# Optimization experiments

Measured on AMD Instinct MI355X. Metric: run time of the kernel, lower is better.

Reference implementation:

```python
import jax, jax.numpy as jnp
import numpy as np
from jax import lax

BLOCKS, LAYERS = 2, 10
RES_CH, DL_CH, OUT_CH, IN_CH, K = 32, 32, 256, 1, 2
B, L = 4, 65536
W_SCALE = 0.05


def conv1d(x, w, b, dilation=1, padding=0):
    # x: [B, Cin, L], w: [Cout, Cin, K], b: [Cout]
    out = lax.conv_general_dilated(
        x, w, window_strides=(1,), padding=[(padding, padding)],
        rhs_dilation=(dilation,), dimension_numbers=('NCH', 'OIH', 'NCH'))
    return out + b[None, :, None]


def setup_inputs() -> dict:
    key = jax.random.key(0)
    ks = jax.random.split(key, 16)
    n = lambda k, shp: jax.random.normal(k, shp, dtype=jnp.float32) * W_SCALE
    inp = {
        'x': jax.random.normal(ks[0], (B, IN_CH, L), dtype=jnp.float32),
        'w_start': n(ks[1], (RES_CH, IN_CH, 1)),
        'b_start': n(ks[2], (RES_CH,)),
        # per-block, per-layer stacked params
        'filt_w': n(ks[3], (BLOCKS, LAYERS, DL_CH, RES_CH, K)),
        'filt_b': n(ks[4], (BLOCKS, LAYERS, DL_CH)),
        'gate_w': n(ks[5], (BLOCKS, LAYERS, DL_CH, RES_CH, K)),
        'gate_b': n(ks[6], (BLOCKS, LAYERS, DL_CH)),
        'res_w': n(ks[7], (BLOCKS, LAYERS, RES_CH, DL_CH, 1)),
        'res_b': n(ks[8], (BLOCKS, LAYERS, RES_CH)),
        'skip_w': n(ks[9], (BLOCKS, LAYERS, RES_CH, DL_CH, 1)),
        'skip_b': n(ks[10], (BLOCKS, LAYERS, RES_CH)),
        'w_end1': n(ks[11], (OUT_CH, RES_CH, 1)),
        'b_end1': n(ks[12], (OUT_CH,)),
        'w_end2': n(ks[13], (OUT_CH, OUT_CH, 1)),
        'b_end2': n(ks[14], (OUT_CH,)),
    }
    return inp


def reference(x, w_start, b_start, filt_w, filt_b, gate_w, gate_b,
              res_w, res_b, skip_w, skip_b, w_end1, b_end1, w_end2, b_end2):
    resid = conv1d(x, w_start, b_start)                    # [B, RES_CH, L]
    skip_total = jnp.zeros_like(resid)
    for blk in range(BLOCKS):
        r = resid
        skip = jnp.zeros_like(r)
        dilation = 1
        for i in range(LAYERS):
            pad = 1 if i == 0 else dilation * (K - 1) // 2
            f = conv1d(r, filt_w[blk, i], filt_b[blk, i], dilation, pad)
            g = conv1d(r, gate_w[blk, i], gate_b[blk, i], dilation, pad)
            if i == 0:  # source slices off the extra trailing sample
                f = f[:, :, :-1]
                g = g[:, :, :-1]
            layer_out = f * g  # NOTE: original forward applies no tanh/sigmoid
            skip = skip + conv1d(layer_out, skip_w[blk, i], skip_b[blk, i])
            r = r + conv1d(layer_out, res_w[blk, i], res_b[blk, i])
            dilation *= 2
        resid = r
        skip_total = skip_total + skip
    out = jax.nn.relu(skip_total)
    out = jax.nn.relu(conv1d(out, w_end1, b_end1))         # [B, OUT_CH, L]
    return conv1d(out, w_end2, b_end2)
```

## Files before the change

kernel.cpp:

```cpp
#include <hip/hip_runtime.h>

typedef unsigned short ushort_t;
typedef __attribute__((ext_vector_type(8))) short bf16x8;
typedef __attribute__((ext_vector_type(4))) float f32x4;

#define NTOK 262144

__device__ __forceinline__ float bf2f(ushort_t u) {
    union { unsigned u; float f; } v; v.u = ((unsigned)u) << 16; return v.f;
}
__device__ __forceinline__ ushort_t f2bf(float f) {
    union { float f; unsigned u; } v; v.f = f;
    unsigned r = 0x7fffu + ((v.u >> 16) & 1u);
    return (ushort_t)((v.u + r) >> 16);
}
__device__ __forceinline__ float ldany(const void* p, long i, int isf32) {
    return isf32 ? ((const float*)p)[i] : bf2f(((const ushort_t*)p)[i]);
}
__device__ __forceinline__ bf16x8 zero8() {
    bf16x8 z = {0,0,0,0,0,0,0,0}; return z;
}
__device__ __forceinline__ void mm3(f32x4& acc, bf16x8 ah, bf16x8 al,
                                    bf16x8 bh, bf16x8 bl) {
    acc = __builtin_amdgcn_mfma_f32_16x16x32_bf16(ah, bh, acc, 0, 0, 0);
    acc = __builtin_amdgcn_mfma_f32_16x16x32_bf16(ah, bl, acc, 0, 0, 0);
    acc = __builtin_amdgcn_mfma_f32_16x16x32_bf16(al, bh, acc, 0, 0, 0);
}
__device__ __forceinline__ void loD2B(f32x4 lo0, f32x4 lo1, int l15, int l4,
                                      bf16x8& bh, bf16x8& bl) {
    #pragma unroll
    for (int j = 0; j < 8; j++) {
        int src = l15 + (((2 * l4 + (j >> 2)) & 3) << 4);
        float v0 = __shfl(lo0[j & 3], src);
        float v1 = __shfl(lo1[j & 3], src);
        float v = (l4 < 2) ? v0 : v1;
        ushort_t h = f2bf(v);
        bh[j] = (short)h;
        bl[j] = (short)f2bf(v - bf2f(h));
    }
}

#define OFF_FB  122880
#define OFF_GB  123520
#define OFF_RB  124160
#define OFF_SB  124800
#define OFF_WST 125440
#define OFF_BST 125472
#define OFF_B1  133696
#define OFF_B2  199488
#define OFF_FLAG 199744
#define SKIP_OFF 262144
#define OFF_W2AH 8650752
#define OFF_W2AL 8683520
#define OFF_W1AH 8716288
#define OFF_W1AL 8720384
#define OFF_FGW  8724480
#define OFF_GGW  8765440
#define OFF_RWH  8806400
#define OFF_SWH  8826880

__device__ __forceinline__ char* rchunk(void* outb, int buf, int b) {
    return (char*)outb + (((long)buf * 32 + (long)b * 8) << 20);
}

__global__ void k_convert(const void* fw, const void* fb,
                          const void* gw, const void* gb,
                          const void* rw, const void* rb,
                          const void* sw, const void* sb,
                          const void* wst, const void* bst,
                          const void* w1, const void* b1,
                          const void* w2, const void* b2,
                          float* W) {
    __shared__ int sh;
    if (threadIdx.x == 0) sh = 0;
    __syncthreads();
    {
        const ushort_t* p = (const ushort_t*)fw;
        int f = 0;
        for (int j = 0; j < 16; j++) {
            ushort_t u = p[threadIdx.x * 16 + j];
            f |= (((u >> 7) & 0xFF) == 0xFF) ? 1 : 0;
        }
        if (f) atomicOr(&sh, 1);
    }
    __syncthreads();
    const int isf32 = sh;
    if (blockIdx.x == 0 && threadIdx.x == 0) W[OFF_FLAG] = (float)isf32;

    int tid = blockIdx.x * blockDim.x + threadIdx.x;
    int stride = gridDim.x * blockDim.x;

    ushort_t* fgp = (ushort_t*)(W + OFF_FGW);
    ushort_t* ggp = (ushort_t*)(W + OFF_GGW);
    ushort_t* rwp = (ushort_t*)(W + OFF_RWH);
    ushort_t* swp = (ushort_t*)(W + OFF_SWH);
    for (int idx = tid; idx < 20480; idx += stride) {
        int wl = idx >> 10;
        int coci = idx & 1023;
        #pragma unroll
        for (int tap = 0; tap < 2; tap++) {
            long base = (long)wl * 4096 + tap * 2048 + coci;
            float v = ldany(fw, (long)idx * 2 + tap, isf32);
            ushort_t h = f2bf(v);
            fgp[base] = h; fgp[base + 1024] = f2bf(v - bf2f(h));
            v = ldany(gw, (long)idx * 2 + tap, isf32);
            h = f2bf(v);
            ggp[base] = h; ggp[base + 1024] = f2bf(v - bf2f(h));
        }
        {
            long base = (long)wl * 2048 + coci;
            float v = ldany(rw, idx, isf32);
            ushort_t h = f2bf(v);
            rwp[base] = h; rwp[base + 1024] = f2bf(v - bf2f(h));
            v = ldany(sw, idx, isf32);
            h = f2bf(v);
            swp[base] = h; swp[base + 1024] = f2bf(v - bf2f(h));
        }
    }
    for (int idx = tid; idx < 640; idx += stride) {
        W[OFF_FB + idx] = ldany(fb, idx, isf32);
        W[OFF_GB + idx] = ldany(gb, idx, isf32);
        W[OFF_RB + idx] = ldany(rb, idx, isf32);
        W[OFF_SB + idx] = ldany(sb, idx, isf32);
    }
    for (int idx = tid; idx < 32; idx += stride) {
        W[OFF_WST + idx] = ldany(wst, idx, isf32);
        W[OFF_BST + idx] = ldany(bst, idx, isf32);
    }
    for (int idx = tid; idx < 256; idx += stride) {
        W[OFF_B1 + idx] = ldany(b1, idx, isf32);
        W[OFF_B2 + idx] = ldany(b2, idx, isf32);
    }
    {
        ushort_t* w2h = (ushort_t*)(W + OFF_W2AH);
        ushort_t* w2l = (ushort_t*)(W + OFF_W2AL);
        for (int idx = tid; idx < 65536; idx += stride) {
            float v = ldany(w2, idx, isf32);
            ushort_t h = f2bf(v);
            w2h[idx] = h;
            w2l[idx] = f2bf(v - bf2f(h));
        }
        ushort_t* w1h = (ushort_t*)(W + OFF_W1AH);
        ushort_t* w1l = (ushort_t*)(W + OFF_W1AL);
        for (int idx = tid; idx < 8192; idx += stride) {
            float v = ldany(w1, idx, isf32);
            ushort_t h = f2bf(v);
            w1h[idx] = h;
            w1l[idx] = f2bf(v - bf2f(h));
        }
    }
}

__global__ __launch_bounds__(256) void k_init(const void* __restrict__ x,
                                              const float* __restrict__ W,
                                              void* __restrict__ outb,
                                              float* __restrict__ skp) {
    int tid = blockIdx.x * blockDim.x + threadIdx.x;
    int b = tid >> 16, l = tid & 65535;
    const int isf32 = (W[OFF_FLAG] > 0.5f) ? 1 : 0;
    float xv = ldany(x, tid, isf32);
    union { uint4 q[4]; unsigned w[16]; } H, L;
    #pragma unroll
    for (int c2 = 0; c2 < 16; c2++) {
        float v0 = W[OFF_WST + c2*2]     * xv + W[OFF_BST + c2*2];
        float v1 = W[OFF_WST + c2*2 + 1] * xv + W[OFF_BST + c2*2 + 1];
        ushort_t h0 = f2bf(v0), h1 = f2bf(v1);
        H.w[c2] = (unsigned)h0 | ((unsigned)h1 << 16);
        L.w[c2] = (unsigned)f2bf(v0 - bf2f(h0)) |
                  ((unsigned)f2bf(v1 - bf2f(h1)) << 16);
    }
    uint4* rp = (uint4*)(rchunk(outb, 0, b) + (long)l * 128);
    #pragma unroll
    for (int q = 0; q < 4; q++) { rp[q] = H.q[q]; rp[4 + q] = L.q[q]; }
    float* sg = skp + ((long)b << 21) + (long)l * 32;
    f32x4 z = {0.f, 0.f, 0.f, 0.f};
    #pragma unroll
    for (int j = 0; j < 8; j++) *(f32x4*)(sg + j * 4) = z;
}

template<int NTW>
__global__ __launch_bounds__(256) void k_pair(const float* __restrict__ W,
                                              void* __restrict__ outb,
                                              float* __restrict__ skp,
                                              int bufin, int bufout,
                                              int wlX, int t0X, int t1X, int TY) {
    constexpr int RTOK = NTW * 64;
    constexpr int RH = NTW * 32 - 128;
    __shared__ __align__(16) char r1[RTOK * 128];
    __shared__ __align__(16) char sxs[256 * 128];
    const int tid = threadIdx.x;
    const int lane = tid & 63;
    const int wv = tid >> 6;
    const int l15 = lane & 15;
    const int l4 = lane >> 4;
    const int b = blockIdx.x >> 8;
    const int lbase = (blockIdx.x & 255) << 8;

    const char* __restrict__ rin = rchunk(outb, bufin, b);
    char* __restrict__ rout      = rchunk(outb, bufout, b);

    {
        const ushort_t* __restrict__ FG  = (const ushort_t*)(W + OFF_FGW) + (long)wlX * 4096;
        const ushort_t* __restrict__ GG  = (const ushort_t*)(W + OFF_GGW) + (long)wlX * 4096;
        const ushort_t* __restrict__ RWH = (const ushort_t*)(W + OFF_RWH) + (long)wlX * 2048;
        const ushort_t* __restrict__ SWH = (const ushort_t*)(W + OFF_SWH) + (long)wlX * 2048;
        bf16x8 afh[2][2], afl[2][2], agh[2][2], agl[2][2];
        #pragma unroll
        for (int tap = 0; tap < 2; tap++)
            #pragma unroll
            for (int mt = 0; mt < 2; mt++) {
                int row = (mt * 16 + l15) * 32 + l4 * 8;
                afh[tap][mt] = *(const bf16x8*)(FG + tap * 2048 + row);
                afl[tap][mt] = *(const bf16x8*)(FG + tap * 2048 + 1024 + row);
                agh[tap][mt] = *(const bf16x8*)(GG + tap * 2048 + row);
                agl[tap][mt] = *(const bf16x8*)(GG + tap * 2048 + 1024 + row);
            }
        bf16x8 ash[2], asl2[2], arh[2], arl[2];
        #pragma unroll
        for (int mt = 0; mt < 2; mt++) {
            int row = (mt * 16 + l15) * 32 + l4 * 8;
            ash[mt]  = *(const bf16x8*)(SWH + row);
            asl2[mt] = *(const bf16x8*)(SWH + 1024 + row);
            arh[mt]  = *(const bf16x8*)(RWH + row);
            arl[mt]  = *(const bf16x8*)(RWH + 1024 + row);
        }
        f32x4 fb2[2], gb2[2], sb4[2], rb4[2];
        #pragma unroll
        for (int mt = 0; mt < 2; mt++) {
            fb2[mt] = *(const f32x4*)(W + OFF_FB + wlX * 32 + mt * 16 + l4 * 4);
            gb2[mt] = *(const f32x4*)(W + OFF_GB + wlX * 32 + mt * 16 + l4 * 4);
            sb4[mt] = *(const f32x4*)(W + OFF_SB + wlX * 32 + mt * 16 + l4 * 4);
            rb4[mt] = *(const f32x4*)(W + OFF_RB + wlX * 32 + mt * 16 + l4 * 4);
        }
        const int offs[2] = {t0X, t1X};
        for (int it = 0; it < NTW; it++) {
            const int rt = wv * NTW + it;
            const int tokl = lbase - RH + rt * 16 + l15;
            f32x4 fa[2] = {fb2[0], fb2[1]};
            f32x4 ga[2] = {gb2[0], gb2[1]};
            #pragma unroll
            for (int tap = 0; tap < 2; tap++) {
                int lt = tokl + offs[tap];
                bf16x8 bh = zero8(), bl = zero8();
                if ((unsigned)lt < 65536u) {
                    const char* rp = rin + (long)lt * 128 + l4 * 16;
                    bh = *(const bf16x8*)rp;
                    bl = *(const bf16x8*)(rp + 64);
                }
                #pragma unroll
                for (int mt = 0; mt < 2; mt++) {
                    mm3(fa[mt], afh[tap][mt], afl[tap][mt], bh, bl);
                    mm3(ga[mt], agh[tap][mt], agl[tap][mt], bh, bl);
                }
            }
            bf16x8 pbh, pbl;
            loD2B(fa[0] * ga[0], fa[1] * ga[1], l15, l4, pbh, pbl);
            f32x4 rdv[2] = {rb4[0], rb4[1]};
            mm3(rdv[0], arh[0], arl[0], pbh, pbl);
            mm3(rdv[1], arh[1], arl[1], pbh, pbl);
            const int reltok = rt * 16 + l15;
            uint2 rxh[2] = {{0u,0u},{0u,0u}}, rxl[2] = {{0u,0u},{0u,0u}};
            if ((unsigned)tokl < 65536u) {
                const char* rp = rin + (long)tokl * 128 + l4 * 8;
                rxh[0] = *(const uint2*)(rp);
                rxh[1] = *(const uint2*)(rp + 32);
                rxl[0] = *(const uint2*)(rp + 64);
                rxl[1] = *(const uint2*)(rp + 96);
            }
            const int sw = (reltok & 7) << 4;
            #pragma unroll
            for (int mt = 0; mt < 2; mt++) {
                float v0 = bf2f((ushort_t)(rxh[mt].x & 0xffffu)) + bf2f((ushort_t)(rxl[mt].x & 0xffffu)) + rdv[mt][0];
                float v1 = bf2f((ushort_t)(rxh[mt].x >> 16))     + bf2f((ushort_t)(rxl[mt].x >> 16))     + rdv[mt][1];
                float v2 = bf2f((ushort_t)(rxh[mt].y & 0xffffu)) + bf2f((ushort_t)(rxl[mt].y & 0xffffu)) + rdv[mt][2];
                float v3 = bf2f((ushort_t)(rxh[mt].y >> 16))     + bf2f((ushort_t)(rxl[mt].y >> 16))     + rdv[mt][3];
                ushort_t h0 = f2bf(v0), h1 = f2bf(v1), h2 = f2bf(v2), h3 = f2bf(v3);
                uint2 ph, pl;
                ph.x = (unsigned)h0 | ((unsigned)h1 << 16);
                ph.y = (unsigned)h2 | ((unsigned)h3 << 16);
                pl.x = (unsigned)f2bf(v0 - bf2f(h0)) | ((unsigned)f2bf(v1 - bf2f(h1)) << 16);
                pl.y = (unsigned)f2bf(v2 - bf2f(h2)) | ((unsigned)f2bf(v3 - bf2f(h3)) << 16);
                *(uint2*)(r1 + ((reltok * 128 + mt * 32 + l4 * 8) ^ sw)) = ph;
                *(uint2*)(r1 + ((reltok * 128 + 64 + mt * 32 + l4 * 8) ^ sw)) = pl;
            }
            const int rel0 = rt * 16 - RH;
            if (rel0 >= 0 && rel0 < 256) {
                f32x4 sd0 = sb4[0], sd1 = sb4[1];
                mm3(sd0, ash[0], asl2[0], pbh, pbl);
                mm3(sd1, ash[1], asl2[1], pbh, pbl);
                const int ct = rel0 + l15;
                const int sws = (ct & 7) << 4;
                *(f32x4*)(sxs + ((ct * 128 + l4 * 16) ^ sws)) = sd0;
                *(f32x4*)(sxs + ((ct * 128 + 64 + l4 * 16) ^ sws)) = sd1;
            }
        }
    }
    __syncthreads();

    {
        const int wlY = wlX + 1;
        const ushort_t* __restrict__ FG  = (const ushort_t*)(W + OFF_FGW) + (long)wlY * 4096;
        const ushort_t* __restrict__ GG  = (const ushort_t*)(W + OFF_GGW) + (long)wlY * 4096;
        const ushort_t* __restrict__ RWH = (const ushort_t*)(W + OFF_RWH) + (long)wlY * 2048;
        const ushort_t* __restrict__ SWH = (const ushort_t*)(W + OFF_SWH) + (long)wlY * 2048;
        bf16x8 afh[2][2], afl[2][2], agh[2][2], agl[2][2];
        #pragma unroll
        for (int tap = 0; tap < 2; tap++)
            #pragma unroll
            for (int mt = 0; mt < 2; mt++) {
                int row = (mt * 16 + l15) * 32 + l4 * 8;
                afh[tap][mt] = *(const bf16x8*)(FG + tap * 2048 + row);
                afl[tap][mt] = *(const bf16x8*)(FG + tap * 2048 + 1024 + row);
                agh[tap][mt] = *(const bf16x8*)(GG + tap * 2048 + row);
                agl[tap][mt] = *(const bf16x8*)(GG + tap * 2048 + 1024 + row);
            }
        bf16x8 ash[2], asl2[2], arh[2], arl[2];
        #pragma unroll
        for (int mt = 0; mt < 2; mt++) {
            int row = (mt * 16 + l15) * 32 + l4 * 8;
            ash[mt]  = *(const bf16x8*)(SWH + row);
            asl2[mt] = *(const bf16x8*)(SWH + 1024 + row);
            arh[mt]  = *(const bf16x8*)(RWH + row);
            arl[mt]  = *(const bf16x8*)(RWH + 1024 + row);
        }
        f32x4 fb2[2], gb2[2], sb4[2], rb4[2];
        #pragma unroll
        for (int mt = 0; mt < 2; mt++) {
            fb2[mt] = *(const f32x4*)(W + OFF_FB + wlY * 32 + mt * 16 + l4 * 4);
            gb2[mt] = *(const f32x4*)(W + OFF_GB + wlY * 32 + mt * 16 + l4 * 4);
            sb4[mt] = *(const f32x4*)(W + OFF_SB + wlY * 32 + mt * 16 + l4 * 4);
            rb4[mt] = *(const f32x4*)(W + OFF_RB + wlY * 32 + mt * 16 + l4 * 4);
        }
        #pragma unroll
        for (int it = 0; it < 4; it++) {
            const int tt = wv * 64 + it * 16 + l15;
            const int tokg = lbase + tt;
            f32x4 fa[2] = {fb2[0], fb2[1]};
            f32x4 ga[2] = {gb2[0], gb2[1]};
            #pragma unroll
            for (int tap = 0; tap < 2; tap++) {
                int dd = tap ? TY : -TY;
                int tg = tokg + dd;
                bf16x8 bh = zero8(), bl = zero8();
                if ((unsigned)tg < 65536u) {
                    int rel = tt + dd + RH;
                    int sw = (rel & 7) << 4;
                    bh = *(const bf16x8*)(r1 + ((rel * 128 + l4 * 16) ^ sw));
                    bl = *(const bf16x8*)(r1 + ((rel * 128 + 64 + l4 * 16) ^ sw));
                }
                #pragma unroll
                for (int mt = 0; mt < 2; mt++) {
                    mm3(fa[mt], afh[tap][mt], afl[tap][mt], bh, bl);
                    mm3(ga[mt], agh[tap][mt], agl[tap][mt], bh, bl);
                }
            }
            bf16x8 pbh, pbl;
            loD2B(fa[0] * ga[0], fa[1] * ga[1], l15, l4, pbh, pbl);
            f32x4 sd0 = sb4[0], sd1 = sb4[1];
            mm3(sd0, ash[0], asl2[0], pbh, pbl);
            mm3(sd1, ash[1], asl2[1], pbh, pbl);
            f32x4 rdv[2] = {rb4[0], rb4[1]};
            mm3(rdv[0], arh[0], arl[0], pbh, pbl);
            mm3(rdv[1], arh[1], arl[1], pbh, pbl);
            {
                const int swc = (tt & 7) << 4;
                f32x4 sx0 = *(const f32x4*)(sxs + ((tt * 128 + l4 * 16) ^ swc));
                f32x4 sx1 = *(const f32x4*)(sxs + ((tt * 128 + 64 + l4 * 16) ^ swc));
                float* sg = skp + ((long)b << 21) + (long)tokg * 32 + l4 * 4;
                *(f32x4*)sg        = *(const f32x4*)sg        + (sd0 + sx0);
                *(f32x4*)(sg + 16) = *(const f32x4*)(sg + 16) + (sd1 + sx1);
            }
            const int relc = tt + RH;
            const int swr = (relc & 7) << 4;
            #pragma unroll
            for (int mt = 0; mt < 2; mt++) {
                uint2 h  = *(const uint2*)(r1 + ((relc * 128 + mt * 32 + l4 * 8) ^ swr));
                uint2 lo = *(const uint2*)(r1 + ((relc * 128 + 64 + mt * 32 + l4 * 8) ^ swr));
                float v0 = bf2f((ushort_t)(h.x & 0xffffu)) + bf2f((ushort_t)(lo.x & 0xffffu)) + rdv[mt][0];
                float v1 = bf2f((ushort_t)(h.x >> 16))     + bf2f((ushort_t)(lo.x >> 16))     + rdv[mt][1];
                float v2 = bf2f((ushort_t)(h.y & 0xffffu)) + bf2f((ushort_t)(lo.y & 0xffffu)) + rdv[mt][2];
                float v3 = bf2f((ushort_t)(h.y >> 16))     + bf2f((ushort_t)(lo.y >> 16))     + rdv[mt][3];
                ushort_t h0 = f2bf(v0), h1 = f2bf(v1), h2 = f2bf(v2), h3 = f2bf(v3);
                uint2 ph, pl;
                ph.x = (unsigned)h0 | ((unsigned)h1 << 16);
                ph.y = (unsigned)h2 | ((unsigned)h3 << 16);
                pl.x = (unsigned)f2bf(v0 - bf2f(h0)) | ((unsigned)f2bf(v1 - bf2f(h1)) << 16);
                pl.y = (unsigned)f2bf(v2 - bf2f(h2)) | ((unsigned)f2bf(v3 - bf2f(h3)) << 16);
                char* op = rout + (long)tokg * 128 + mt * 32 + l4 * 8;
                *(uint2*)op        = ph;
                *(uint2*)(op + 64) = pl;
            }
        }
    }
}

__global__ __launch_bounds__(512, 4) void k_final(const float* __restrict__ W,
                                                  const float* __restrict__ skp,
                                                  void* __restrict__ outv) {
    __shared__ ushort_t h1s[128 * 256];
    const int tid = threadIdx.x;
    const int lane = tid & 63;
    const int wv = tid >> 6;
    const int wm = wv & 3;
    const int wn = wv >> 2;
    const int l15 = lane & 15;
    const int l4 = lane >> 4;
    const int isf32 = (W[OFF_FLAG] > 0.5f) ? 1 : 0;
    const int tokbase = blockIdx.x * 128 + wn * 64;

    const ushort_t* __restrict__ W1AH = (const ushort_t*)(W + OFF_W1AH);
    const ushort_t* __restrict__ W1AL = (const ushort_t*)(W + OFF_W1AL);
    const ushort_t* __restrict__ W2AH = (const ushort_t*)(W + OFF_W2AH);
    const ushort_t* __restrict__ W2AL = (const ushort_t*)(W + OFF_W2AL);

    bf16x8 bhi[4], blo[4];
    #pragma unroll
    for (int nt = 0; nt < 4; nt++) {
        int tok = tokbase + nt * 16 + l15;
        int bb = tok >> 16, ll = tok & 65535;
        const float* __restrict__ sk = skp + ((long)bb << 21) + (long)ll * 32 + l4 * 8;
        f32x4 u0 = *(const f32x4*)(sk);
        f32x4 u1 = *(const f32x4*)(sk + 4);
        bf16x8 h, o_;
        #pragma unroll
        for (int j = 0; j < 8; j++) {
            float v = (j < 4) ? u0[j] : u1[j - 4];
            v = v > 0.f ? v : 0.f;
            ushort_t hh = f2bf(v);
            h[j] = (short)hh;
            o_[j] = (short)f2bf(v - bf2f(hh));
        }
        bhi[nt] = h; blo[nt] = o_;
    }

    #pragma unroll
    for (int mt = 0; mt < 4; mt++) {
        int o0 = wm * 64 + mt * 16;
        const bf16x8 a_hi = *(const bf16x8*)(W1AH + (o0 + l15) * 32 + l4 * 8);
        const bf16x8 a_lo = *(const bf16x8*)(W1AL + (o0 + l15) * 32 + l4 * 8);
        f32x4 bias;
        #pragma unroll
        for (int r = 0; r < 4; r++) bias[r] = W[OFF_B1 + o0 + l4 * 4 + r];
        #pragma unroll
        for (int nt = 0; nt < 4; nt++) {
            f32x4 acc = bias;
            acc = __builtin_amdgcn_mfma_f32_16x16x32_bf16(a_hi, bhi[nt], acc, 0, 0, 0);
            acc = __builtin_amdgcn_mfma_f32_16x16x32_bf16(a_hi, blo[nt], acc, 0, 0, 0);
            acc = __builtin_amdgcn_mfma_f32_16x16x32_bf16(a_lo, bhi[nt], acc, 0, 0, 0);
            int ltk = wn * 64 + nt * 16 + l15;
            int ci0 = o0 + l4 * 4;
            float v0 = acc[0] > 0.f ? acc[0] : 0.f;
            float v1 = acc[1] > 0.f ? acc[1] : 0.f;
            float v2 = acc[2] > 0.f ? acc[2] : 0.f;
            float v3 = acc[3] > 0.f ? acc[3] : 0.f;
            uint2 pk;
            pk.x = (unsigned)f2bf(v0) | ((unsigned)f2bf(v1) << 16);
            pk.y = (unsigned)f2bf(v2) | ((unsigned)f2bf(v3) << 16);
            int byteoff = (ltk << 9) + (ci0 << 1);
            byteoff ^= (ltk & 7) << 4;
            *(uint2*)((char*)h1s + byteoff) = pk;
        }
    }
    __syncthreads();

    f32x4 acc[4][4];
    #pragma unroll
    for (int mt = 0; mt < 4; mt++) {
        int m0 = wm * 64 + mt * 16 + l4 * 4;
        #pragma unroll
        for (int r = 0; r < 4; r++) {
            float bv = W[OFF_B2 + m0 + r];
            #pragma unroll
            for (int nt = 0; nt < 4; nt++) acc[mt][nt][r] = bv;
        }
    }
    #pragma unroll 2
    for (int ks = 0; ks < 8; ks++) {
        bf16x8 bf[4];
        #pragma unroll
        for (int nt = 0; nt < 4; nt++) {
            int ltk = wn * 64 + nt * 16 + l15;
            int byteoff = (ltk << 9) + (ks << 6) + (l4 << 4);
            byteoff ^= (ltk & 7) << 4;
            bf[nt] = *(const bf16x8*)((const char*)h1s + byteoff);
        }
        #pragma unroll
        for (int mt = 0; mt < 4; mt++) {
            int o = wm * 64 + mt * 16 + l15;
            const bf16x8 a_hi = *(const bf16x8*)(W2AH + o * 256 + ks * 32 + l4 * 8);
            #pragma unroll
            for (int nt = 0; nt < 4; nt++)
                acc[mt][nt] = __builtin_amdgcn_mfma_f32_16x16x32_bf16(a_hi, bf[nt], acc[mt][nt], 0, 0, 0);
            const bf16x8 a_lo = *(const bf16x8*)(W2AL + o * 256 + ks * 32 + l4 * 8);
            #pragma unroll
            for (int nt = 0; nt < 4; nt++)
                acc[mt][nt] = __builtin_amdgcn_mfma_f32_16x16x32_bf16(a_lo, bf[nt], acc[mt][nt], 0, 0, 0);
        }
    }

    #pragma unroll
    for (int nt = 0; nt < 4; nt++) {
        int tok = tokbase + nt * 16 + l15;
        int bb = tok >> 16, ll = tok & 65535;
        #pragma unroll
        for (int mt = 0; mt < 4; mt++) {
            int m0 = wm * 64 + mt * 16 + l4 * 4;
            if (isf32) {
                float* ob = (float*)outv + ((long)bb << 24) + ((long)m0 << 16) + ll;
                #pragma unroll
                for (int r = 0; r < 4; r++) ob[(long)r << 16] = acc[mt][nt][r];
            } else {
                ushort_t* ob = (ushort_t*)outv + ((long)bb << 24) + ((long)m0 << 16) + ll;
                #pragma unroll
                for (int r = 0; r < 4; r++) ob[(long)r << 16] = f2bf(acc[mt][nt][r]);
            }
        }
    }
}

extern "C" void kernel_launch(void* const* d_in, const int* in_sizes, int n_in,
                              void* d_out, int out_size, void* d_ws, size_t ws_size,
                              hipStream_t stream) {
    const void* x    = d_in[0];
    const void* wst  = d_in[1];
    const void* bst  = d_in[2];
    const void* fw   = d_in[3];
    const void* fb   = d_in[4];
    const void* gw   = d_in[5];
    const void* gb   = d_in[6];
    const void* rw   = d_in[7];
    const void* rb   = d_in[8];
    const void* sw   = d_in[9];
    const void* sb   = d_in[10];
    const void* w1   = d_in[11];
    const void* b1   = d_in[12];
    const void* w2   = d_in[13];
    const void* b2   = d_in[14];

    float* W   = (float*)d_ws;
    float* skp = W + SKIP_OFF;

    k_convert<<<64, 256, 0, stream>>>(fw, fb, gw, gb, rw, rb, sw, sb,
                                      wst, bst, w1, b1, w2, b2, W);
    k_init<<<NTOK / 256, 256, 0, stream>>>(x, W, d_out, skp);

    int cur = 0;
    for (int blk = 0; blk < 2; blk++) {
        int base = blk * 10;
        k_pair<5><<<1024, 256, 0, stream>>>(W, d_out, skp, cur, cur ^ 1, base + 0, -1,   0,   1); cur ^= 1;
        k_pair<5><<<1024, 256, 0, stream>>>(W, d_out, skp, cur, cur ^ 1, base + 2, -2,   2,   4); cur ^= 1;
        k_pair<5><<<1024, 256, 0, stream>>>(W, d_out, skp, cur, cur ^ 1, base + 4, -8,   8,  16); cur ^= 1;
        k_pair<6><<<1024, 256, 0, stream>>>(W, d_out, skp, cur, cur ^ 1, base + 6, -32,  32,  64); cur ^= 1;
        k_pair<12><<<1024, 256, 0, stream>>>(W, d_out, skp, cur, cur ^ 1, base + 8, -128, 128, 256); cur ^= 1;
    }
    k_final<<<NTOK / 128, 512, 0, stream>>>(W, skp, d_out);
}
```

Baseline: 1.106 ms.

## Fuse start conv into first layer pair, drop shuffles, widen last pair

```diff
diff --git a/kernel.cpp b/kernel.cpp
--- a/kernel.cpp
+++ b/kernel.cpp
@@ -26,17 +26,15 @@
     acc = __builtin_amdgcn_mfma_f32_16x16x32_bf16(ah, bl, acc, 0, 0, 0);
     acc = __builtin_amdgcn_mfma_f32_16x16x32_bf16(al, bh, acc, 0, 0, 0);
 }
-__device__ __forceinline__ void loD2B(f32x4 lo0, f32x4 lo1, int l15, int l4,
-                                      bf16x8& bh, bf16x8& bl) {
+__device__ __forceinline__ void packP(f32x4 p0, f32x4 p1, bf16x8& bh, bf16x8& bl) {
     #pragma unroll
-    for (int j = 0; j < 8; j++) {
-        int src = l15 + (((2 * l4 + (j >> 2)) & 3) << 4);
-        float v0 = __shfl(lo0[j & 3], src);
-        float v1 = __shfl(lo1[j & 3], src);
-        float v = (l4 < 2) ? v0 : v1;
-        ushort_t h = f2bf(v);
-        bh[j] = (short)h;
-        bl[j] = (short)f2bf(v - bf2f(h));
+    for (int r = 0; r < 4; r++) {
+        float v0 = p0[r], v1 = p1[r];
+        ushort_t h0 = f2bf(v0), h1 = f2bf(v1);
+        bh[r]     = (short)h0;
+        bh[r + 4] = (short)h1;
+        bl[r]     = (short)f2bf(v0 - bf2f(h0));
+        bl[r + 4] = (short)f2bf(v1 - bf2f(h1));
     }
 }
 
@@ -108,7 +106,9 @@
             ggp[base] = h; ggp[base + 1024] = f2bf(v - bf2f(h));
         }
         {
-            long base = (long)wl * 2048 + coci;
+            int ci = coci & 31, co = coci >> 5;
+            int p = ((ci >> 2) & 3) * 8 + ((ci >> 4) & 1) * 4 + (ci & 3);
+            long base = (long)wl * 2048 + co * 32 + p;
             float v = ldany(rw, idx, isf32);
             ushort_t h = f2bf(v);
             rwp[base] = h; rwp[base + 1024] = f2bf(v - bf2f(h));
@@ -151,41 +151,16 @@
     }
 }
 
-__global__ __launch_bounds__(256) void k_init(const void* __restrict__ x,
-                                              const float* __restrict__ W,
-                                              void* __restrict__ outb,
-                                              float* __restrict__ skp) {
-    int tid = blockIdx.x * blockDim.x + threadIdx.x;
-    int b = tid >> 16, l = tid & 65535;
-    const int isf32 = (W[OFF_FLAG] > 0.5f) ? 1 : 0;
-    float xv = ldany(x, tid, isf32);
-    union { uint4 q[4]; unsigned w[16]; } H, L;
-    #pragma unroll
-    for (int c2 = 0; c2 < 16; c2++) {
-        float v0 = W[OFF_WST + c2*2]     * xv + W[OFF_BST + c2*2];
-        float v1 = W[OFF_WST + c2*2 + 1] * xv + W[OFF_BST + c2*2 + 1];
-        ushort_t h0 = f2bf(v0), h1 = f2bf(v1);
-        H.w[c2] = (unsigned)h0 | ((unsigned)h1 << 16);
-        L.w[c2] = (unsigned)f2bf(v0 - bf2f(h0)) |
-                  ((unsigned)f2bf(v1 - bf2f(h1)) << 16);
-    }
-    uint4* rp = (uint4*)(rchunk(outb, 0, b) + (long)l * 128);
-    #pragma unroll
-    for (int q = 0; q < 4; q++) { rp[q] = H.q[q]; rp[4 + q] = L.q[q]; }
-    float* sg = skp + ((long)b << 21) + (long)l * 32;
-    f32x4 z = {0.f, 0.f, 0.f, 0.f};
-    #pragma unroll
-    for (int j = 0; j < 8; j++) *(f32x4*)(sg + j * 4) = z;
-}
-
-template<int NTW>
-__global__ __launch_bounds__(256) void k_pair(const float* __restrict__ W,
-                                              void* __restrict__ outb,
-                                              float* __restrict__ skp,
-                                              int bufin, int bufout,
-                                              int wlX, int t0X, int t1X, int TY) {
-    constexpr int RTOK = NTW * 64;
-    constexpr int RH = NTW * 32 - 128;
+template<int NTX, int NWAVE, bool FIRST>
+__global__ __launch_bounds__(NWAVE * 64) void k_pair(const float* __restrict__ W,
+                                                     const void* __restrict__ xin,
+                                                     void* __restrict__ outb,
+                                                     float* __restrict__ skp,
+                                                     int bufin, int bufout,
+                                                     int wlX, int t0X, int t1X, int TY) {
+    constexpr int RTOK = NTX * NWAVE * 16;
+    constexpr int RH = (RTOK - 256) / 2;
+    constexpr int NCT = 16 / NWAVE;
     __shared__ __align__(16) char r1[RTOK * 128];
     __shared__ __align__(16) char sxs[256 * 128];
     const int tid = threadIdx.x;
@@ -198,6 +173,7 @@
 
     const char* __restrict__ rin = rchunk(outb, bufin, b);
     char* __restrict__ rout      = rchunk(outb, bufout, b);
+    const int isf32 = FIRST ? ((W[OFF_FLAG] > 0.5f) ? 1 : 0) : 0;
 
     {
         const ushort_t* __restrict__ FG  = (const ushort_t*)(W + OFF_FGW) + (long)wlX * 4096;
@@ -232,20 +208,42 @@
             sb4[mt] = *(const f32x4*)(W + OFF_SB + wlX * 32 + mt * 16 + l4 * 4);
             rb4[mt] = *(const f32x4*)(W + OFF_RB + wlX * 32 + mt * 16 + l4 * 4);
         }
-        const int offs[2] = {t0X, t1X};
-        for (int it = 0; it < NTW; it++) {
-            const int rt = wv * NTW + it;
+        float wstS[8], bstS[8], wstD[8], bstD[8];
+        if (FIRST) {
+            #pragma unroll
+            for (int j = 0; j < 8; j++) {
+                wstS[j] = W[OFF_WST + l4 * 8 + j];
+                bstS[j] = W[OFF_BST + l4 * 8 + j];
+                int c = (j >> 2) * 16 + l4 * 4 + (j & 3);
+                wstD[j] = W[OFF_WST + c];
+                bstD[j] = W[OFF_BST + c];
+            }
+        }
+        const int offs2[2] = {t0X, t1X};
+        for (int it = 0; it < NTX; it++) {
+            const int rt = wv * NTX + it;
             const int tokl = lbase - RH + rt * 16 + l15;
             f32x4 fa[2] = {fb2[0], fb2[1]};
             f32x4 ga[2] = {gb2[0], gb2[1]};
             #pragma unroll
             for (int tap = 0; tap < 2; tap++) {
-                int lt = tokl + offs[tap];
+                int lt = tokl + offs2[tap];
                 bf16x8 bh = zero8(), bl = zero8();
                 if ((unsigned)lt < 65536u) {
-                    const char* rp = rin + (long)lt * 128 + l4 * 16;
-                    bh = *(const bf16x8*)rp;
-                    bl = *(const bf16x8*)(rp + 64);
+                    if (FIRST) {
+                        float xv = ldany(xin, ((long)b << 16) + lt, isf32);
+                        #pragma unroll
+                        for (int j = 0; j < 8; j++) {
+                            float v = wstS[j] * xv + bstS[j];
+                            ushort_t h = f2bf(v);
+                            bh[j] = (short)h;
+                            bl[j] = (short)f2bf(v - bf2f(h));
+                        }
+                    } else {
+                        const char* rp = rin + (long)lt * 128 + l4 * 16;
+                        bh = *(const bf16x8*)rp;
+                        bl = *(const bf16x8*)(rp + 64);
+                    }
                 }
                 #pragma unroll
                 for (int mt = 0; mt < 2; mt++) {
@@ -254,26 +252,49 @@
                 }
             }
             bf16x8 pbh, pbl;
-            loD2B(fa[0] * ga[0], fa[1] * ga[1], l15, l4, pbh, pbl);
+            packP(fa[0] * ga[0], fa[1] * ga[1], pbh, pbl);
             f32x4 rdv[2] = {rb4[0], rb4[1]};
             mm3(rdv[0], arh[0], arl[0], pbh, pbl);
             mm3(rdv[1], arh[1], arl[1], pbh, pbl);
+            float rx[8];
+            if (FIRST) {
+                if ((unsigned)tokl < 65536u) {
+                    float xv = ldany(xin, ((long)b << 16) + tokl, isf32);
+                    #pragma unroll
+                    for (int j = 0; j < 8; j++) {
+                        float v = wstD[j] * xv + bstD[j];
+                        ushort_t h = f2bf(v);
+                        rx[j] = bf2f(h) + bf2f(f2bf(v - bf2f(h)));
+                    }
+                } else {
+                    #pragma unroll
+                    for (int j = 0; j < 8; j++) rx[j] = 0.f;
+                }
+            } else {
+                uint2 rxh[2] = {{0u,0u},{0u,0u}}, rxl[2] = {{0u,0u},{0u,0u}};
+                if ((unsigned)tokl < 65536u) {
+                    const char* rp = rin + (long)tokl * 128 + l4 * 8;
+                    rxh[0] = *(const uint2*)(rp);
+                    rxh[1] = *(const uint2*)(rp + 32);
+                    rxl[0] = *(const uint2*)(rp + 64);
+                    rxl[1] = *(const uint2*)(rp + 96);
+                }
+                #pragma unroll
+                for (int mt = 0; mt < 2; mt++) {
+                    rx[mt*4+0] = bf2f((ushort_t)(rxh[mt].x & 0xffffu)) + bf2f((ushort_t)(rxl[mt].x & 0xffffu));
+                    rx[mt*4+1] = bf2f((ushort_t)(rxh[mt].x >> 16))     + bf2f((ushort_t)(rxl[mt].x >> 16));
+                    rx[mt*4+2] = bf2f((ushort_t)(rxh[mt].y & 0xffffu)) + bf2f((ushort_t)(rxl[mt].y & 0xffffu));
+                    rx[mt*4+3] = bf2f((ushort_t)(rxh[mt].y >> 16))     + bf2f((ushort_t)(rxl[mt].y >> 16));
+                }
+            }
             const int reltok = rt * 16 + l15;
-            uint2 rxh[2] = {{0u,0u},{0u,0u}}, rxl[2] = {{0u,0u},{0u,0u}};
-            if ((unsigned)tokl < 65536u) {
-                const char* rp = rin + (long)tokl * 128 + l4 * 8;
-                rxh[0] = *(const uint2*)(rp);
-                rxh[1] = *(const uint2*)(rp + 32);
-                rxl[0] = *(const uint2*)(rp + 64);
-                rxl[1] = *(const uint2*)(rp + 96);
-            }
             const int sw = (reltok & 7) << 4;
             #pragma unroll
             for (int mt = 0; mt < 2; mt++) {
-                float v0 = bf2f((ushort_t)(rxh[mt].x & 0xffffu)) + bf2f((ushort_t)(rxl[mt].x & 0xffffu)) + rdv[mt][0];
-                float v1 = bf2f((ushort_t)(rxh[mt].x >> 16))     + bf2f((ushort_t)(rxl[mt].x >> 16))     + rdv[mt][1];
-                float v2 = bf2f((ushort_t)(rxh[mt].y & 0xffffu)) + bf2f((ushort_t)(rxl[mt].y & 0xffffu)) + rdv[mt][2];
-                float v3 = bf2f((ushort_t)(rxh[mt].y >> 16))     + bf2f((ushort_t)(rxl[mt].y >> 16))     + rdv[mt][3];
+                float v0 = rx[mt*4+0] + rdv[mt][0];
+                float v1 = rx[mt*4+1] + rdv[mt][1];
+                float v2 = rx[mt*4+2] + rdv[mt][2];
+                float v3 = rx[mt*4+3] + rdv[mt][3];
                 ushort_t h0 = f2bf(v0), h1 = f2bf(v1), h2 = f2bf(v2), h3 = f2bf(v3);
                 uint2 ph, pl;
                 ph.x = (unsigned)h0 | ((unsigned)h1 << 16);
@@ -332,8 +353,8 @@
             rb4[mt] = *(const f32x4*)(W + OFF_RB + wlY * 32 + mt * 16 + l4 * 4);
         }
         #pragma unroll
-        for (int it = 0; it < 4; it++) {
-            const int tt = wv * 64 + it * 16 + l15;
+        for (int it = 0; it < NCT; it++) {
+            const int tt = (wv * NCT + it) * 16 + l15;
             const int tokg = lbase + tt;
             f32x4 fa[2] = {fb2[0], fb2[1]};
             f32x4 ga[2] = {gb2[0], gb2[1]};
@@ -355,7 +376,7 @@
                 }
             }
             bf16x8 pbh, pbl;
-            loD2B(fa[0] * ga[0], fa[1] * ga[1], l15, l4, pbh, pbl);
+            packP(fa[0] * ga[0], fa[1] * ga[1], pbh, pbl);
             f32x4 sd0 = sb4[0], sd1 = sb4[1];
             mm3(sd0, ash[0], asl2[0], pbh, pbl);
             mm3(sd1, ash[1], asl2[1], pbh, pbl);
@@ -367,8 +388,13 @@
                 f32x4 sx0 = *(const f32x4*)(sxs + ((tt * 128 + l4 * 16) ^ swc));
                 f32x4 sx1 = *(const f32x4*)(sxs + ((tt * 128 + 64 + l4 * 16) ^ swc));
                 float* sg = skp + ((long)b << 21) + (long)tokg * 32 + l4 * 4;
-                *(f32x4*)sg        = *(const f32x4*)sg        + (sd0 + sx0);
-                *(f32x4*)(sg + 16) = *(const f32x4*)(sg + 16) + (sd1 + sx1);
+                if (FIRST) {
+                    *(f32x4*)sg        = sd0 + sx0;
+                    *(f32x4*)(sg + 16) = sd1 + sx1;
+                } else {
+                    *(f32x4*)sg        = *(const f32x4*)sg        + (sd0 + sx0);
+                    *(f32x4*)(sg + 16) = *(const f32x4*)(sg + 16) + (sd1 + sx1);
+                }
             }
             const int relc = tt + RH;
             const int swr = (relc & 7) << 4;
@@ -542,16 +568,27 @@
 
     k_convert<<<64, 256, 0, stream>>>(fw, fb, gw, gb, rw, rb, sw, sb,
                                       wst, bst, w1, b1, w2, b2, W);
-    k_init<<<NTOK / 256, 256, 0, stream>>>(x, W, d_out, skp);
 
     int cur = 0;
     for (int blk = 0; blk < 2; blk++) {
         int base = blk * 10;
-        k_pair<5><<<1024, 256, 0, stream>>>(W, d_out, skp, cur, cur ^ 1, base + 0, -1,   0,   1); cur ^= 1;
-        k_pair<5><<<1024, 256, 0, stream>>>(W, d_out, skp, cur, cur ^ 1, base + 2, -2,   2,   4); cur ^= 1;
-        k_pair<5><<<1024, 256, 0, stream>>>(W, d_out, skp, cur, cur ^ 1, base + 4, -8,   8,  16); cur ^= 1;
-        k_pair<6><<<1024, 256, 0, stream>>>(W, d_out, skp, cur, cur ^ 1, base + 6, -32,  32,  64); cur ^= 1;
-        k_pair<12><<<1024, 256, 0, stream>>>(W, d_out, skp, cur, cur ^ 1, base + 8, -128, 128, 256); cur ^= 1;
+        if (blk == 0) {
+            k_pair<5, 4, true><<<1024, 256, 0, stream>>>(W, x, d_out, skp, 0, 0,
+                                                         base + 0, -1, 0, 1);
+            cur = 0;
+        } else {
+            k_pair<5, 4, false><<<1024, 256, 0, stream>>>(W, x, d_out, skp, cur, cur ^ 1,
+                                                          base + 0, -1, 0, 1);
+            cur ^= 1;
+        }
+        k_pair<5, 4, false><<<1024, 256, 0, stream>>>(W, x, d_out, skp, cur, cur ^ 1,
+                                                      base + 2, -2, 2, 4);   cur ^= 1;
+        k_pair<5, 4, false><<<1024, 256, 0, stream>>>(W, x, d_out, skp, cur, cur ^ 1,
+                                                      base + 4, -8, 8, 16);  cur ^= 1;
+        k_pair<6, 4, false><<<1024, 256, 0, stream>>>(W, x, d_out, skp, cur, cur ^ 1,
+                                                      base + 6, -32, 32, 64); cur ^= 1;
+        k_pair<6, 8, false><<<1024, 512, 0, stream>>>(W, x, d_out, skp, cur, cur ^ 1,
+                                                      base + 8, -128, 128, 256); cur ^= 1;
     }
     k_final<<<NTOK / 128, 512, 0, stream>>>(W, skp, d_out);
 }
```

Measured after the change: 1.029 ms. 1.07x faster.
